# Optimization experiments

Hardware: AMD Instinct MI355X
Metric: run time of the kernel (lower is better)

## Reference

```python
import jax, jax.numpy as jnp
import numpy as np

EMBED_DIM = 64
GAMMA = 1.0
N_X = 8192
N_Y = 8192


def _self_attention(inputs, W_q, W_k):
    # inputs: [n, d]; W_q, W_k: [d, d]
    q = inputs @ W_q
    k = inputs @ W_k
    scores = jax.nn.softmax(q @ k.T / jnp.sqrt(jnp.float32(EMBED_DIM)), axis=-1)  # [n, n]
    return scores @ inputs  # [n, d]


def setup_inputs() -> dict:
    key = jax.random.key(0)
    k1, k2, k3, k4 = jax.random.split(key, 4)
    return {
        "rotation_params": jax.random.normal(k1, (EMBED_DIM, EMBED_DIM), dtype=jnp.float32),
        "entangle_params": jax.random.normal(k2, (EMBED_DIM, EMBED_DIM), dtype=jnp.float32),
        "x": jax.random.normal(k3, (N_X, EMBED_DIM), dtype=jnp.float32),
        "y": jax.random.normal(k4, (N_Y, EMBED_DIM), dtype=jnp.float32),
    }


def reference(rotation_params, entangle_params, x, y):
    x_att = _self_attention(x, rotation_params, entangle_params)  # [n_x, d]
    y_att = _self_attention(y, rotation_params, entangle_params)  # [n_y, d]
    # Pairwise squared distances, vectorizing the original per-pair loop.
    diff = x_att[:, None, :] - y_att[None, :, :]  # [n_x, n_y, d]
    sq = jnp.sum(diff * diff, axis=-1)  # [n_x, n_y]
    return jnp.exp(-GAMMA * sq)
```

## Files before the change

kernel.cpp:

```cpp
#include <hip/hip_runtime.h>
#include <math.h>

#define N 8192
#define D 64
#define KS 4
#define LOG2E 1.4426950408889634f

typedef _Float16 half_t;
typedef _Float16 f16x8 __attribute__((ext_vector_type(8)));
typedef _Float16 f16x4 __attribute__((ext_vector_type(4)));
typedef float f32x4 __attribute__((ext_vector_type(4)));

#define MFMA32(a, b, c) __builtin_amdgcn_mfma_f32_16x16x32_f16((a), (b), (c), 0, 0, 0)

#define SPLIT(v, H, L) { half_t _h = (half_t)(v); (H) = _h; (L) = (half_t)((v) - (float)_h); }


__global__ __launch_bounds__(256) void proj_kernel(
    const float* __restrict__ Wq, const float* __restrict__ Wk,
    const float* __restrict__ X, const float* __restrict__ Y,
    half_t* __restrict__ Qfx, half_t* __restrict__ Qfy,
    half_t* __restrict__ Kfx, half_t* __restrict__ Kfy)
{
    __shared__ float sWq[64][64];
    __shared__ float sWk[64][64];
    __shared__ float sIn[16][64];
    const int t = threadIdx.x;
#pragma unroll
    for (int p = 0; p < 16; ++p) {
        int idx = p * 256 + t;
        sWq[idx >> 6][idx & 63] = Wq[idx];
        sWk[idx >> 6][idx & 63] = Wk[idx];
    }
    const int R0 = blockIdx.x * 16;
    const float* src; half_t* dqf; half_t* dkf; int r0;
    if (R0 < N) { src = X; dqf = Qfx; dkf = Kfx; r0 = R0; }
    else        { src = Y; dqf = Qfy; dkf = Kfy; r0 = R0 - N; }
#pragma unroll
    for (int p = 0; p < 4; ++p) {
        int idx = p * 256 + t;
        sIn[idx >> 6][idx & 63] = src[(size_t)r0 * D + idx];
    }
    __syncthreads();
    const int c = t & 63;
    const int rb = t >> 6;
    const int ksi = c >> 5, quadi = (c >> 3) & 3, j = c & 7;
#pragma unroll
    for (int rr = 0; rr < 4; ++rr) {
        int r = rr * 4 + rb;
        float aq = 0.f, ak = 0.f;
#pragma unroll
        for (int k = 0; k < 64; ++k) {
            float xv = sIn[r][k];
            aq = fmaf(xv, sWq[k][c], aq);
            ak = fmaf(xv, sWk[k][c], ak);
        }
        aq *= (0.125f * LOG2E);
        int rg = r0 + r;
        int tile = rg >> 5, tau = (rg >> 4) & 1, c16l = rg & 15;
        size_t idx = (size_t)tile * 4096 + ksi * 2048 + tau * 1024
                   + (quadi * 16 + c16l) * 8 + j;
        half_t qhh = (half_t)aq;
        dqf[idx]       = qhh;
        dqf[idx + 512] = (half_t)(aq - (float)qhh);
        half_t khh = (half_t)ak;
        dkf[idx]       = khh;
        dkf[idx + 512] = (half_t)(ak - (float)khh);
    }
}

__global__ __launch_bounds__(256) void ztprep_kernel(
    const float* __restrict__ X, const float* __restrict__ Y,
    half_t* __restrict__ Zfx, half_t* __restrict__ Zfy)
{
    const int t = threadIdx.x;
    const int tile = blockIdx.x;
    const float* src = blockIdx.y ? Y : X;
    half_t* dst = blockIdx.y ? Zfy : Zfx;
    const int dt = t >> 6, lane = t & 63;
    const int quad = lane >> 4, c16 = lane & 15;
    f16x8 h;
#pragma unroll
    for (int j = 0; j < 8; ++j)
        h[j] = (half_t)src[(size_t)(tile * 32 + quad * 8 + j) * D + dt * 16 + c16];
    *(f16x8*)&dst[(size_t)tile * 2048 + dt * 512 + lane * 8] = h;
}

__global__ __launch_bounds__(256, 2) void attn_kernel(
    const half_t* __restrict__ Qfx, const half_t* __restrict__ Qfy,
    const half_t* __restrict__ Kfx, const half_t* __restrict__ Kfy,
    const half_t* __restrict__ Zfx, const half_t* __restrict__ Zfy,
    half_t* __restrict__ Opart, float* __restrict__ mpart, float* __restrict__ lpart)
{
    const int side = blockIdx.y;
    const half_t* Qf = side ? Qfy : Qfx;
    const half_t* Kf = side ? Kfy : Kfx;
    const half_t* Zf = side ? Zfy : Zfx;
    const int t = threadIdx.x, w = t >> 6, lane = t & 63;
    const int c16 = lane & 15, quad = lane >> 4;
    const int q0 = blockIdx.x * 128 + w * 32;
    const int tile0 = blockIdx.z * (N / KS / 32);
    const int ITERS = (N / KS) / 32;

    __shared__ half_t Pbuf[4][32][40];
    half_t (*Phi)[40] = Pbuf[w];

    f16x8 qh[2][2], ql[2][2];
    {
        const half_t* qb = Qf + (size_t)(q0 >> 5) * 4096 + lane * 8;
#pragma unroll
        for (int ks = 0; ks < 2; ++ks)
#pragma unroll
            for (int qg = 0; qg < 2; ++qg) {
                qh[qg][ks] = *(const f16x8*)&qb[ks * 2048 + qg * 1024];
                ql[qg][ks] = *(const f16x8*)&qb[ks * 2048 + qg * 1024 + 512];
            }
    }

    f32x4 ot[4][2] = {};
    f32x4 lacc[2] = {};
    float m_run[2] = {-INFINITY, -INFINITY};
    f16x8 ones;
#pragma unroll
    for (int i = 0; i < 8; ++i) ones[i] = (half_t)1.0f;

    f16x8 kAh[2][2], kAl[2][2], kBh[2][2], kBl[2][2];
    f32x4 stA[2][2], stB[2][2];

    auto loadK = [&](int tile, f16x8 (&kh)[2][2], f16x8 (&kl)[2][2]) {
        const half_t* b = Kf + (size_t)tile * 4096 + lane * 8;
#pragma unroll
        for (int ks = 0; ks < 2; ++ks)
#pragma unroll
            for (int tau = 0; tau < 2; ++tau) {
                kh[ks][tau] = *(const f16x8*)&b[ks * 2048 + tau * 1024];
                kl[ks][tau] = *(const f16x8*)&b[ks * 2048 + tau * 1024 + 512];
            }
    };
    auto doS = [&](f32x4 (&st)[2][2], f16x8 (&kh)[2][2], f16x8 (&kl)[2][2]) {
        const f32x4 zero = {};
#pragma unroll
        for (int qg = 0; qg < 2; ++qg)
#pragma unroll
            for (int tau = 0; tau < 2; ++tau) st[qg][tau] = zero;
#pragma unroll
        for (int ks = 0; ks < 2; ++ks)
#pragma unroll
            for (int tau = 0; tau < 2; ++tau)
#pragma unroll
                for (int qg = 0; qg < 2; ++qg) {
                    st[qg][tau] = MFMA32(kh[ks][tau], qh[qg][ks], st[qg][tau]);
                    st[qg][tau] = MFMA32(kh[ks][tau], ql[qg][ks], st[qg][tau]);
                    st[qg][tau] = MFMA32(kl[ks][tau], qh[qg][ks], st[qg][tau]);
                }
    };

    auto body = [&](int tt, f32x4 (&stCur)[2][2], f32x4 (&stNext)[2][2],
                    f16x8 (&kNh)[2][2], f16x8 (&kNl)[2][2],
                    f16x8 (&kRh)[2][2], f16x8 (&kRl)[2][2]) {
        if (tt + 1 < ITERS) doS(stNext, kNh, kNl);
        if (tt + 2 < ITERS) loadK(tile0 + tt + 2, kRh, kRl);
        const half_t* zb = Zf + (size_t)(tile0 + tt) * 2048 + lane * 8;
        f16x8 zh[4];
#pragma unroll
        for (int dt = 0; dt < 4; ++dt)
            zh[dt] = *(const f16x8*)&zb[dt * 512];
#pragma unroll
        for (int qg = 0; qg < 2; ++qg) {
            float mt = fmaxf(fmaxf(fmaxf(stCur[qg][0][0], stCur[qg][0][1]),
                                   fmaxf(stCur[qg][0][2], stCur[qg][0][3])),
                             fmaxf(fmaxf(stCur[qg][1][0], stCur[qg][1][1]),
                                   fmaxf(stCur[qg][1][2], stCur[qg][1][3])));
            mt = fmaxf(mt, __shfl_xor(mt, 16));
            mt = fmaxf(mt, __shfl_xor(mt, 32));
            float mn = fmaxf(m_run[qg], mt);
            float al = exp2f(m_run[qg] - mn);
            m_run[qg] = mn;
#pragma unroll
            for (int tau = 0; tau < 2; ++tau) {
                f16x4 h4;
#pragma unroll
                for (int r = 0; r < 4; ++r)
                    h4[r] = (half_t)exp2f(stCur[qg][tau][r] - mn);
                *(f16x4*)&Phi[16 * qg + c16][16 * tau + 4 * quad] = h4;
            }
            lacc[qg] *= al;
#pragma unroll
            for (int dt = 0; dt < 4; ++dt) ot[dt][qg] *= al;
        }
        f16x8 pbh[2];
#pragma unroll
        for (int qg = 0; qg < 2; ++qg)
            pbh[qg] = *(const f16x8*)&Phi[16 * qg + c16][quad * 8];
#pragma unroll
        for (int dt = 0; dt < 4; ++dt)
#pragma unroll
            for (int qg = 0; qg < 2; ++qg)
                ot[dt][qg] = MFMA32(zh[dt], pbh[qg], ot[dt][qg]);
#pragma unroll
        for (int qg = 0; qg < 2; ++qg)
            lacc[qg] = MFMA32(ones, pbh[qg], lacc[qg]);
    };

    loadK(tile0, kAh, kAl);
    doS(stA, kAh, kAl);
    if (ITERS > 1) loadK(tile0 + 1, kBh, kBl);
#pragma unroll 1
    for (int tt = 0; tt < ITERS; tt += 2) {
        body(tt,     stA, stB, kBh, kBl, kAh, kAl);
        body(tt + 1, stB, stA, kAh, kAl, kBh, kBl);
    }

    const size_t obase = (size_t)(side * KS + blockIdx.z) * N;
#pragma unroll
    for (int qg = 0; qg < 2; ++qg) {
        int q = q0 + 16 * qg + c16;
#pragma unroll
        for (int dt = 0; dt < 4; ++dt) {
            f16x4 o4;
#pragma unroll
            for (int r = 0; r < 4; ++r) o4[r] = (half_t)ot[dt][qg][r];
            *(f16x4*)&Opart[(obase + q) * D + 16 * dt + 4 * quad] = o4;
        }
        if (quad == 0) {
            mpart[obase + q] = m_run[qg];
            lpart[obase + q] = lacc[qg][0];
        }
    }
}

__global__ __launch_bounds__(256) void combine_kernel(
    const half_t* __restrict__ Opart, const float* __restrict__ mpart,
    const float* __restrict__ lpart,
    half_t* __restrict__ Xf, half_t* __restrict__ Yf,
    float* __restrict__ n2x, float* __restrict__ n2y)
{
    const int side = blockIdx.y;
    const int q = blockIdx.x * 16 + (threadIdx.x >> 4);
    const int d4 = (threadIdx.x & 15) * 4;
    float m[KS], l[KS];
#pragma unroll
    for (int s = 0; s < KS; ++s) {
        size_t b = (size_t)(side * KS + s) * N + q;
        m[s] = mpart[b]; l[s] = lpart[b];
    }
    float M = -INFINITY;
#pragma unroll
    for (int s = 0; s < KS; ++s) M = fmaxf(M, m[s]);
    float L = 0.f;
    f32x4 o = {0.f, 0.f, 0.f, 0.f};
#pragma unroll
    for (int s = 0; s < KS; ++s) {
        float sc = exp2f(m[s] - M);
        L += l[s] * sc;
        f16x4 p4 = *(const f16x4*)&Opart[((size_t)(side * KS + s) * N + q) * D + d4];
#pragma unroll
        for (int i = 0; i < 4; ++i) o[i] = fmaf((float)p4[i], sc, o[i]);
    }
    const float oscale = (side ? 1.0f : 2.0f * LOG2E) / L;
    f16x4 h4;
#pragma unroll
    for (int i = 0; i < 4; ++i) h4[i] = (half_t)(o[i] * oscale);
    float sq = 0.f;
#pragma unroll
    for (int i = 0; i < 4; ++i) { float hv = (float)h4[i]; sq = fmaf(hv, hv, sq); }
#pragma unroll
    for (int off = 1; off < 16; off <<= 1) sq += __shfl_xor(sq, off);
    half_t* dst = side ? Yf : Xf;
    float*  n2  = side ? n2y : n2x;
    if ((threadIdx.x & 15) == 0)
        n2[q] = side ? sq * LOG2E : sq * (0.25f / LOG2E);
    const int tile16 = q >> 4, c16l = q & 15;
    const int ksi = d4 >> 5, quadi = (d4 >> 3) & 3, j0 = d4 & 7;
    *(f16x4*)&dst[(size_t)tile16 * 1024 + ksi * 512 + (quadi * 16 + c16l) * 8 + j0] = h4;
}

__global__ __launch_bounds__(256, 4) void rbf_kernel(
    const half_t* __restrict__ Xf, const half_t* __restrict__ Yf,
    const float* __restrict__ n2x, const float* __restrict__ n2y,
    float* __restrict__ out)
{
    const int t = threadIdx.x, w = t >> 6, lane = t & 63;
    const int c16 = lane & 15, quad = lane >> 4;
    const int X0 = blockIdx.y * 128 + (w >> 1) * 64;
    const int Y0 = blockIdx.x * 128 + (w & 1) * 64;
    float ny[4];
    f32x4 nx4[4];
#pragma unroll
    for (int yt = 0; yt < 4; ++yt) ny[yt] = n2y[Y0 + 16 * yt + c16];
#pragma unroll
    for (int xt = 0; xt < 4; ++xt)
        nx4[xt] = *(const f32x4*)&n2x[X0 + 16 * xt + 4 * quad];

    const half_t* Xb = Xf + lane * 8;
    const half_t* Yb = Yf + lane * 8;
    f32x4 acc[4][4] = {};
#pragma unroll
    for (int ks = 0; ks < 2; ++ks) {
        f16x8 bh[4];
#pragma unroll
        for (int yt = 0; yt < 4; ++yt)
            bh[yt] = *(const f16x8*)&Yb[(size_t)((Y0 >> 4) + yt) * 1024 + ks * 512];
#pragma unroll
        for (int xt = 0; xt < 4; ++xt) {
            f16x8 ah = *(const f16x8*)&Xb[(size_t)((X0 >> 4) + xt) * 1024 + ks * 512];
#pragma unroll
            for (int yt = 0; yt < 4; ++yt)
                acc[xt][yt] = MFMA32(ah, bh[yt], acc[xt][yt]);
        }
    }
#pragma unroll
    for (int xt = 0; xt < 4; ++xt)
#pragma unroll
        for (int r = 0; r < 4; ++r) {
            int xr = X0 + 16 * xt + 4 * quad + r;
            float nx = nx4[xt][r];
#pragma unroll
            for (int yt = 0; yt < 4; ++yt) {
                float v = exp2f(acc[xt][yt][r] - nx - ny[yt]);
                out[(size_t)xr * N + Y0 + 16 * yt + c16] = v;
            }
        }
}

extern "C" void kernel_launch(void* const* d_in, const int* in_sizes, int n_in,
                              void* d_out, int out_size, void* d_ws, size_t ws_size,
                              hipStream_t stream) {
    const float* Wq = (const float*)d_in[0];
    const float* Wk = (const float*)d_in[1];
    const float* x  = (const float*)d_in[2];
    const float* y  = (const float*)d_in[3];
    float* out = (float*)d_out;

    char* p = (char*)d_ws;
    size_t used = 0;
    auto alloc = [&](size_t bytes) -> void* {
        void* r = (void*)(p + used);
        used += (bytes + 255) & ~(size_t)255;
        return r;
    };
    half_t* Qfx = (half_t*)alloc((size_t)N * D * 2 * 2);
    half_t* Qfy = (half_t*)alloc((size_t)N * D * 2 * 2);
    half_t* Kfx = (half_t*)alloc((size_t)N * D * 2 * 2);
    half_t* Kfy = (half_t*)alloc((size_t)N * D * 2 * 2);
    half_t* Zfx = (half_t*)alloc((size_t)N * D * 2);
    half_t* Zfy = (half_t*)alloc((size_t)N * D * 2);
    half_t* Xf  = (half_t*)alloc((size_t)N * D * 2);
    half_t* Yf  = (half_t*)alloc((size_t)N * D * 2);
    float*  n2x = (float*) alloc((size_t)N * 4);
    float*  n2y = (float*) alloc((size_t)N * 4);
    half_t* Opart = (half_t*)alloc((size_t)2 * KS * N * D * 2);
    float*  mpart = (float*) alloc((size_t)2 * KS * N * 4);
    float*  lpart = (float*) alloc((size_t)2 * KS * N * 4);

    proj_kernel<<<dim3(2 * N / 16), 256, 0, stream>>>(Wq, Wk, x, y,
                                                      Qfx, Qfy, Kfx, Kfy);
    ztprep_kernel<<<dim3(N / 32, 2), 256, 0, stream>>>(x, y, Zfx, Zfy);
    attn_kernel<<<dim3(N / 128, 2, KS), 256, 0, stream>>>(
        Qfx, Qfy, Kfx, Kfy, Zfx, Zfy, Opart, mpart, lpart);
    combine_kernel<<<dim3(N / 16, 2), 256, 0, stream>>>(
        Opart, mpart, lpart, Xf, Yf, n2x, n2y);
    rbf_kernel<<<dim3(N / 128, N / 128), 256, 0, stream>>>(Xf, Yf, n2x, n2y, out);
}
```

Measured before the change: 390.1 us.

## Vectorize RBF output stores, enlarge attention blocks, add MFMA priority hints

The RBF kernel swaps its MFMA operand order so each lane holds four consecutive output columns. It then writes the 256MB output with 16-byte nontemporal vector stores instead of scalar strided stores. The attention kernel moves to 512-thread blocks of 8 waves and raises wave priority around its MFMA sections. The projection kernel reorders its loops to reuse each weight load across four rows. The RBF store change targets the dominant write-bandwidth cost. The other changes are smaller scheduling and reuse tweaks that could shift occupancy.

Result: slower. 408.7 us (+4.8%).

```diff
diff --git a/kernel.cpp b/kernel.cpp
--- a/kernel.cpp
+++ b/kernel.cpp
@@ -12,8 +12,6 @@
 typedef float f32x4 __attribute__((ext_vector_type(4)));
 
 #define MFMA32(a, b, c) __builtin_amdgcn_mfma_f32_16x16x32_f16((a), (b), (c), 0, 0, 0)
-
-#define SPLIT(v, H, L) { half_t _h = (half_t)(v); (H) = _h; (L) = (half_t)((v) - (float)_h); }
 
 
 __global__ __launch_bounds__(256) void proj_kernel(
@@ -45,27 +43,33 @@
     const int c = t & 63;
     const int rb = t >> 6;
     const int ksi = c >> 5, quadi = (c >> 3) & 3, j = c & 7;
+    float aq[4] = {0.f, 0.f, 0.f, 0.f};
+    float ak[4] = {0.f, 0.f, 0.f, 0.f};
+#pragma unroll
+    for (int k = 0; k < 64; ++k) {
+        float wqv = sWq[k][c];
+        float wkv = sWk[k][c];
+#pragma unroll
+        for (int rr = 0; rr < 4; ++rr) {
+            float xv = sIn[rr * 4 + rb][k];
+            aq[rr] = fmaf(xv, wqv, aq[rr]);
+            ak[rr] = fmaf(xv, wkv, ak[rr]);
+        }
+    }
 #pragma unroll
     for (int rr = 0; rr < 4; ++rr) {
-        int r = rr * 4 + rb;
-        float aq = 0.f, ak = 0.f;
-#pragma unroll
-        for (int k = 0; k < 64; ++k) {
-            float xv = sIn[r][k];
-            aq = fmaf(xv, sWq[k][c], aq);
-            ak = fmaf(xv, sWk[k][c], ak);
-        }
-        aq *= (0.125f * LOG2E);
-        int rg = r0 + r;
+        float aqv = aq[rr] * (0.125f * LOG2E);
+        float akv = ak[rr];
+        int rg = r0 + rr * 4 + rb;
         int tile = rg >> 5, tau = (rg >> 4) & 1, c16l = rg & 15;
         size_t idx = (size_t)tile * 4096 + ksi * 2048 + tau * 1024
                    + (quadi * 16 + c16l) * 8 + j;
-        half_t qhh = (half_t)aq;
+        half_t qhh = (half_t)aqv;
         dqf[idx]       = qhh;
-        dqf[idx + 512] = (half_t)(aq - (float)qhh);
-        half_t khh = (half_t)ak;
+        dqf[idx + 512] = (half_t)(aqv - (float)qhh);
+        half_t khh = (half_t)akv;
         dkf[idx]       = khh;
-        dkf[idx + 512] = (half_t)(ak - (float)khh);
+        dkf[idx + 512] = (half_t)(akv - (float)khh);
     }
 }
 
@@ -86,7 +90,7 @@
     *(f16x8*)&dst[(size_t)tile * 2048 + dt * 512 + lane * 8] = h;
 }
 
-__global__ __launch_bounds__(256, 2) void attn_kernel(
+__global__ __launch_bounds__(512, 1) void attn_kernel(
     const half_t* __restrict__ Qfx, const half_t* __restrict__ Qfy,
     const half_t* __restrict__ Kfx, const half_t* __restrict__ Kfy,
     const half_t* __restrict__ Zfx, const half_t* __restrict__ Zfy,
@@ -98,11 +102,11 @@
     const half_t* Zf = side ? Zfy : Zfx;
     const int t = threadIdx.x, w = t >> 6, lane = t & 63;
     const int c16 = lane & 15, quad = lane >> 4;
-    const int q0 = blockIdx.x * 128 + w * 32;
+    const int q0 = blockIdx.x * 256 + w * 32;
     const int tile0 = blockIdx.z * (N / KS / 32);
     const int ITERS = (N / KS) / 32;
 
-    __shared__ half_t Pbuf[4][32][40];
+    __shared__ half_t Pbuf[8][32][40];
     half_t (*Phi)[40] = Pbuf[w];
 
     f16x8 qh[2][2], ql[2][2];
@@ -143,6 +147,7 @@
         for (int qg = 0; qg < 2; ++qg)
 #pragma unroll
             for (int tau = 0; tau < 2; ++tau) st[qg][tau] = zero;
+        __builtin_amdgcn_s_setprio(1);
 #pragma unroll
         for (int ks = 0; ks < 2; ++ks)
 #pragma unroll
@@ -153,6 +158,7 @@
                     st[qg][tau] = MFMA32(kh[ks][tau], ql[qg][ks], st[qg][tau]);
                     st[qg][tau] = MFMA32(kl[ks][tau], qh[qg][ks], st[qg][tau]);
                 }
+        __builtin_amdgcn_s_setprio(0);
     };
 
     auto body = [&](int tt, f32x4 (&stCur)[2][2], f32x4 (&stNext)[2][2],
@@ -192,6 +198,7 @@
 #pragma unroll
         for (int qg = 0; qg < 2; ++qg)
             pbh[qg] = *(const f16x8*)&Phi[16 * qg + c16][quad * 8];
+        __builtin_amdgcn_s_setprio(1);
 #pragma unroll
         for (int dt = 0; dt < 4; ++dt)
 #pragma unroll
@@ -200,6 +207,7 @@
 #pragma unroll
         for (int qg = 0; qg < 2; ++qg)
             lacc[qg] = MFMA32(ones, pbh[qg], lacc[qg]);
+        __builtin_amdgcn_s_setprio(0);
     };
 
     loadK(tile0, kAh, kAl);
@@ -284,43 +292,44 @@
     const int c16 = lane & 15, quad = lane >> 4;
     const int X0 = blockIdx.y * 128 + (w >> 1) * 64;
     const int Y0 = blockIdx.x * 128 + (w & 1) * 64;
-    float ny[4];
-    f32x4 nx4[4];
-#pragma unroll
-    for (int yt = 0; yt < 4; ++yt) ny[yt] = n2y[Y0 + 16 * yt + c16];
-#pragma unroll
-    for (int xt = 0; xt < 4; ++xt)
-        nx4[xt] = *(const f32x4*)&n2x[X0 + 16 * xt + 4 * quad];
+    float nx[4];
+    f32x4 ny4[4];
+#pragma unroll
+    for (int xt = 0; xt < 4; ++xt) nx[xt] = n2x[X0 + 16 * xt + c16];
+#pragma unroll
+    for (int yt = 0; yt < 4; ++yt)
+        ny4[yt] = *(const f32x4*)&n2y[Y0 + 16 * yt + 4 * quad];
 
     const half_t* Xb = Xf + lane * 8;
     const half_t* Yb = Yf + lane * 8;
     f32x4 acc[4][4] = {};
 #pragma unroll
     for (int ks = 0; ks < 2; ++ks) {
-        f16x8 bh[4];
-#pragma unroll
-        for (int yt = 0; yt < 4; ++yt)
-            bh[yt] = *(const f16x8*)&Yb[(size_t)((Y0 >> 4) + yt) * 1024 + ks * 512];
-#pragma unroll
-        for (int xt = 0; xt < 4; ++xt) {
-            f16x8 ah = *(const f16x8*)&Xb[(size_t)((X0 >> 4) + xt) * 1024 + ks * 512];
-#pragma unroll
-            for (int yt = 0; yt < 4; ++yt)
-                acc[xt][yt] = MFMA32(ah, bh[yt], acc[xt][yt]);
-        }
-    }
-#pragma unroll
-    for (int xt = 0; xt < 4; ++xt)
-#pragma unroll
-        for (int r = 0; r < 4; ++r) {
-            int xr = X0 + 16 * xt + 4 * quad + r;
-            float nx = nx4[xt][r];
-#pragma unroll
-            for (int yt = 0; yt < 4; ++yt) {
-                float v = exp2f(acc[xt][yt][r] - nx - ny[yt]);
-                out[(size_t)xr * N + Y0 + 16 * yt + c16] = v;
-            }
-        }
+        f16x8 ax[4];
+#pragma unroll
+        for (int xt = 0; xt < 4; ++xt)
+            ax[xt] = *(const f16x8*)&Xb[(size_t)((X0 >> 4) + xt) * 1024 + ks * 512];
+#pragma unroll
+        for (int yt = 0; yt < 4; ++yt) {
+            f16x8 ay = *(const f16x8*)&Yb[(size_t)((Y0 >> 4) + yt) * 1024 + ks * 512];
+#pragma unroll
+            for (int xt = 0; xt < 4; ++xt)
+                acc[yt][xt] = MFMA32(ay, ax[xt], acc[yt][xt]);
+        }
+    }
+#pragma unroll
+    for (int xt = 0; xt < 4; ++xt) {
+        const int xr = X0 + 16 * xt + c16;
+        float* rowp = out + (size_t)xr * N + Y0 + 4 * quad;
+#pragma unroll
+        for (int yt = 0; yt < 4; ++yt) {
+            f32x4 v;
+#pragma unroll
+            for (int r = 0; r < 4; ++r)
+                v[r] = exp2f(acc[yt][xt][r] - nx[xt] - ny4[yt][r]);
+            __builtin_nontemporal_store(v, (f32x4*)(rowp + 16 * yt));
+        }
+    }
 }
 
 extern "C" void kernel_launch(void* const* d_in, const int* in_sizes, int n_in,
@@ -356,7 +365,7 @@
     proj_kernel<<<dim3(2 * N / 16), 256, 0, stream>>>(Wq, Wk, x, y,
                                                       Qfx, Qfy, Kfx, Kfy);
     ztprep_kernel<<<dim3(N / 32, 2), 256, 0, stream>>>(x, y, Zfx, Zfy);
-    attn_kernel<<<dim3(N / 128, 2, KS), 256, 0, stream>>>(
+    attn_kernel<<<dim3(N / 256, 2, KS), 512, 0, stream>>>(
         Qfx, Qfy, Kfx, Kfy, Zfx, Zfy, Opart, mpart, lpart);
     combine_kernel<<<dim3(N / 16, 2), 256, 0, stream>>>(
         Opart, mpart, lpart, Xf, Yf, n2x, n2y);
```
